# Performance work log

Hardware: AMD Instinct MI355X
Metric: run time of the kernel (lower is better)

## Reference

```python
import math
import jax, jax.numpy as jnp
import numpy as np

EPS = 1e-12
NHEAD = 12
HEAD_DIM = 64  # d_model // nhead = 768 // 12


def setup_inputs() -> dict:
    key = jax.random.key(0)
    ks = jax.random.split(key, 8)
    L, D, H = 12, 768, 2048
    B, S = 8, 1024
    std = 0.02
    return {
        "x": jax.random.normal(ks[0], (B, S, D), jnp.float32),
        "wq": jax.random.normal(ks[1], (L, D, D), jnp.float32) * std,
        "wk": jax.random.normal(ks[2], (L, D, D), jnp.float32) * std,
        "wv": jax.random.normal(ks[3], (L, D, D), jnp.float32) * std,
        "wo": jax.random.normal(ks[4], (L, D, D), jnp.float32) * std,
        "w1": jax.random.normal(ks[5], (L, H, D), jnp.float32) * std,
        "w2": jax.random.normal(ks[6], (L, D, H), jnp.float32) * std,
        "attn_norm_w": jnp.ones((L, D), jnp.float32),
        "ffn_norm_w": jnp.ones((L, D), jnp.float32),
    }


def _rmsnorm(x, w):
    # x * rsqrt(mean(x^2) + eps) * w
    return x * jax.lax.rsqrt(jnp.mean(x * x, axis=-1, keepdims=True) + EPS) * w


def _block(x, params):
    wq, wk, wv, wo, w1, w2, anw, fnw = params
    B, S, D = x.shape
    # --- attention (manual matmul-softmax-matmul, fp32 softmax) ---
    xn = _rmsnorm(x, anw)
    q = jnp.einsum('bsd,ed->bse', xn, wq).reshape(B, S, NHEAD, HEAD_DIM)
    k = jnp.einsum('bsd,ed->bse', xn, wk).reshape(B, S, NHEAD, HEAD_DIM)
    v = jnp.einsum('bsd,ed->bse', xn, wv).reshape(B, S, NHEAD, HEAD_DIM)
    scores = jnp.einsum('bqhd,bkhd->bhqk', q, k) / math.sqrt(HEAD_DIM)
    probs = jax.nn.softmax(scores.astype(jnp.float32), axis=-1).astype(x.dtype)
    attn = jnp.einsum('bhqk,bkhd->bqhd', probs, v).reshape(B, S, D)
    h = x + jnp.einsum('bsd,ed->bse', attn, wo)
    # --- FFN: w2(silu(w1(h_norm))) ---
    hn = _rmsnorm(h, fnw)
    ff = jnp.einsum('bsh,dh->bsd', jax.nn.silu(jnp.einsum('bsd,hd->bsh', hn, w1)), w2)
    return h + ff


def reference(x, wq, wk, wv, wo, w1, w2, attn_norm_w, ffn_norm_w):
    def step(carry, p):
        return _block(carry, p), None
    out, _ = jax.lax.scan(step, x, (wq, wk, wv, wo, w1, w2, attn_norm_w, ffn_norm_w))
    return out
```

## Files before the change

kernel.cpp:

```cpp
#include <hip/hip_runtime.h>
#include <stdint.h>

typedef unsigned short u16;
typedef unsigned int u32;
typedef __bf16 bf16x8 __attribute__((ext_vector_type(8)));
typedef __bf16 bf16x4 __attribute__((ext_vector_type(4)));
typedef float f32x4 __attribute__((ext_vector_type(4)));

__device__ __forceinline__ u16 f2bf(float f) {
  u32 u = __builtin_bit_cast(u32, f);
  u32 r = (u + 0x7FFFu + ((u >> 16) & 1u)) >> 16;
  return (u16)r;
}

__global__ __launch_bounds__(256)
void convert_w(const float* __restrict__ wq, const float* __restrict__ wk,
               const float* __restrict__ wv, const float* __restrict__ wo,
               const float* __restrict__ w1, const float* __restrict__ w2,
               u16* __restrict__ out) {
  size_t i = ((size_t)blockIdx.x * 256 + threadIdx.x) * 4;
  if (i >= 5505024) return;
  const float* src; size_t off;
  if (i < 589824)       { src = wq; off = i; }
  else if (i < 1179648) { src = wk; off = i - 589824; }
  else if (i < 1769472) { src = wv; off = i - 1179648; }
  else if (i < 2359296) { src = wo; off = i - 1769472; }
  else if (i < 3932160) { src = w1; off = i - 2359296; }
  else                  { src = w2; off = i - 3932160; }
  float4 v = *(const float4*)(src + off);
  u32 lo = (u32)f2bf(v.x) | ((u32)f2bf(v.y) << 16);
  u32 hi = (u32)f2bf(v.z) | ((u32)f2bf(v.w) << 16);
  *(uint2*)(out + i) = make_uint2(lo, hi);
}

__device__ __forceinline__ void rn_store4(u16* p, float4 v, float4 w, float sc) {
  u32 lo = (u32)f2bf(v.x * sc * w.x) | ((u32)f2bf(v.y * sc * w.y) << 16);
  u32 hi = (u32)f2bf(v.z * sc * w.z) | ((u32)f2bf(v.w * sc * w.w) << 16);
  *(uint2*)p = make_uint2(lo, hi);
}

__global__ __launch_bounds__(256)
void rmsnorm_k(const float* __restrict__ x, const float* __restrict__ w,
               u16* __restrict__ out) {
  const int tok = (blockIdx.x << 2) + (threadIdx.x >> 6);
  const int l = threadIdx.x & 63;
  const float* xr = x + (size_t)tok * 768;
  float4 v0 = *(const float4*)(xr + l * 4);
  float4 v1 = *(const float4*)(xr + 256 + l * 4);
  float4 v2 = *(const float4*)(xr + 512 + l * 4);
  float ss = v0.x*v0.x + v0.y*v0.y + v0.z*v0.z + v0.w*v0.w
           + v1.x*v1.x + v1.y*v1.y + v1.z*v1.z + v1.w*v1.w
           + v2.x*v2.x + v2.y*v2.y + v2.z*v2.z + v2.w*v2.w;
  ss += __shfl_xor(ss, 1);  ss += __shfl_xor(ss, 2);  ss += __shfl_xor(ss, 4);
  ss += __shfl_xor(ss, 8);  ss += __shfl_xor(ss, 16); ss += __shfl_xor(ss, 32);
  float sc = rsqrtf(ss * (1.f / 768.f) + 1e-12f);
  float4 w0 = *(const float4*)(w + l * 4);
  float4 w1v = *(const float4*)(w + 256 + l * 4);
  float4 w2v = *(const float4*)(w + 512 + l * 4);
  u16* o = out + (size_t)tok * 768;
  rn_store4(o + l * 4, v0, w0, sc);
  rn_store4(o + 256 + l * 4, v1, w1v, sc);
  rn_store4(o + 512 + l * 4, v2, w2v, sc);
}

#define GEMM_CORE(A_, W_, K_, m0_, n0_)                                             \
  for (int kt = 0; kt < (K_); kt += 64) {                                           \
    __syncthreads();                                                                \
    _Pragma("unroll")                                                               \
    for (int ii = 0; ii < 4; ++ii) {                                                \
      int issue = (w << 2) + ii;                                                    \
      int r = (issue << 3) + (l >> 3);                                              \
      int c = (l & 7) ^ (r & 7);                                                    \
      __builtin_amdgcn_global_load_lds((A_) + (size_t)((m0_) + r) * (K_) + kt + c * 8, \
                                       As + issue * 512, 16, 0, 0);                 \
      __builtin_amdgcn_global_load_lds((W_) + (size_t)((n0_) + r) * (K_) + kt + c * 8, \
                                       Ws + issue * 512, 16, 0, 0);                 \
    }                                                                               \
    __syncthreads();                                                                \
    _Pragma("unroll")                                                               \
    for (int kc = 0; kc < 2; ++kc) {                                                \
      int chunk = lg + (kc << 2);                                                   \
      bf16x8 af[4], bfr[4];                                                         \
      _Pragma("unroll")                                                             \
      for (int i = 0; i < 4; ++i) {                                                 \
        int mr = (wm << 6) + (i << 4) + ll;                                         \
        af[i] = *(const bf16x8*)((const char*)As + mr * 128 + ((chunk ^ (mr & 7)) << 4)); \
        int nr = (wn << 6) + (i << 4) + ll;                                         \
        bfr[i] = *(const bf16x8*)((const char*)Ws + nr * 128 + ((chunk ^ (nr & 7)) << 4)); \
      }                                                                             \
      _Pragma("unroll")                                                             \
      for (int i = 0; i < 4; ++i)                                                   \
        _Pragma("unroll")                                                           \
        for (int j = 0; j < 4; ++j)                                                 \
          acc[i][j] = __builtin_amdgcn_mfma_f32_16x16x32_bf16(af[i], bfr[j], acc[i][j], 0, 0, 0); \
    }                                                                               \
  }

template<int EP>
__global__ __launch_bounds__(256, 2)
void gemm_bt(const u16* __restrict__ A, const u16* __restrict__ W,
             void* __restrict__ outp, const float* __restrict__ Res,
             int M, int N, int K) {
  __shared__ __align__(16) u16 As[128 * 64];
  __shared__ __align__(16) u16 Ws[128 * 64];
  const int tid = threadIdx.x;
  const int w = tid >> 6, l = tid & 63;
  const int lg = l >> 4, ll = l & 15;
  const int ntiles = N >> 7;
  const int mt = blockIdx.x / ntiles, nt = blockIdx.x - mt * ntiles;
  const int m0 = mt << 7, n0 = nt << 7;
  const int wm = w >> 1, wn = w & 1;

  const f32x4 fz = {0.f, 0.f, 0.f, 0.f};
  f32x4 acc[4][4];
#pragma unroll
  for (int i = 0; i < 4; ++i)
#pragma unroll
    for (int j = 0; j < 4; ++j) acc[i][j] = fz;

  GEMM_CORE(A, W, K, m0, n0)

  const int g4 = lg << 2;
#pragma unroll
  for (int i = 0; i < 4; ++i) {
#pragma unroll
    for (int j = 0; j < 4; ++j) {
      int row0 = m0 + (wm << 6) + (i << 4) + g4;
      int col = n0 + (wn << 6) + (j << 4) + ll;
      f32x4 v = acc[i][j];
      if (EP == 0) {
        u16* o = (u16*)outp;
#pragma unroll
        for (int e = 0; e < 4; ++e) o[(size_t)(row0 + e) * N + col] = f2bf(v[e]);
      } else if (EP == 1) {
        float* o = (float*)outp;
#pragma unroll
        for (int e = 0; e < 4; ++e) {
          size_t idx = (size_t)(row0 + e) * N + col;
          o[idx] = Res[idx] + v[e];
        }
      } else {
        u16* o = (u16*)outp;
#pragma unroll
        for (int e = 0; e < 4; ++e) {
          float xx = v[e];
          o[(size_t)(row0 + e) * N + col] = f2bf(xx / (1.f + __expf(-xx)));
        }
      }
    }
  }
}

__global__ __launch_bounds__(256, 4)
void gemm_bt64(const u16* __restrict__ A, const u16* __restrict__ W,
               float* __restrict__ outp, const float* __restrict__ Res,
               int M, int N, int K) {
  __shared__ __align__(16) u16 As[64 * 64];
  __shared__ __align__(16) u16 Ws[128 * 64];
  const int tid = threadIdx.x;
  const int w = tid >> 6, l = tid & 63;
  const int lg = l >> 4, ll = l & 15;
  const int ntiles = N >> 7;
  const int mt = blockIdx.x / ntiles, nt = blockIdx.x - mt * ntiles;
  const int m0 = mt << 6, n0 = nt << 7;
  const int wm = w >> 1, wn = w & 1;

  const f32x4 fz = {0.f, 0.f, 0.f, 0.f};
  f32x4 acc[2][4];
#pragma unroll
  for (int i = 0; i < 2; ++i)
#pragma unroll
    for (int j = 0; j < 4; ++j) acc[i][j] = fz;

  for (int kt = 0; kt < K; kt += 64) {
    __syncthreads();
#pragma unroll
    for (int ii = 0; ii < 6; ++ii) {
      int issue = w * 6 + ii;
      if (issue < 8) {
        int r = (issue << 3) + (l >> 3);
        int c = (l & 7) ^ (r & 7);
        __builtin_amdgcn_global_load_lds(A + (size_t)(m0 + r) * K + kt + c * 8,
                                         As + issue * 512, 16, 0, 0);
      } else {
        int is2 = issue - 8;
        int r = (is2 << 3) + (l >> 3);
        int c = (l & 7) ^ (r & 7);
        __builtin_amdgcn_global_load_lds(W + (size_t)(n0 + r) * K + kt + c * 8,
                                         Ws + is2 * 512, 16, 0, 0);
      }
    }
    __syncthreads();
#pragma unroll
    for (int kc = 0; kc < 2; ++kc) {
      int chunk = lg + (kc << 2);
      bf16x8 af[2], bfr[4];
#pragma unroll
      for (int i = 0; i < 2; ++i) {
        int mr = (wm << 5) + (i << 4) + ll;
        af[i] = *(const bf16x8*)((const char*)As + mr * 128 + ((chunk ^ (mr & 7)) << 4));
      }
#pragma unroll
      for (int j = 0; j < 4; ++j) {
        int nr = (wn << 6) + (j << 4) + ll;
        bfr[j] = *(const bf16x8*)((const char*)Ws + nr * 128 + ((chunk ^ (nr & 7)) << 4));
      }
#pragma unroll
      for (int i = 0; i < 2; ++i)
#pragma unroll
        for (int j = 0; j < 4; ++j)
          acc[i][j] = __builtin_amdgcn_mfma_f32_16x16x32_bf16(af[i], bfr[j], acc[i][j], 0, 0, 0);
    }
  }

  const int g4 = lg << 2;
#pragma unroll
  for (int i = 0; i < 2; ++i) {
#pragma unroll
    for (int j = 0; j < 4; ++j) {
      int row0 = m0 + (wm << 5) + (i << 4) + g4;
      int col = n0 + (wn << 6) + (j << 4) + ll;
      f32x4 v = acc[i][j];
#pragma unroll
      for (int e = 0; e < 4; ++e) {
        size_t idx = (size_t)(row0 + e) * N + col;
        outp[idx] = Res[idx] + v[e];
      }
    }
  }
}

__global__ __launch_bounds__(256, 2)
void gemm_qkv(const u16* __restrict__ A, const u16* __restrict__ W,
              u16* __restrict__ Qo, u16* __restrict__ Ko, u16* __restrict__ Vo) {
  __shared__ __align__(16) u16 As[128 * 64];
  __shared__ __align__(16) u16 Ws[128 * 64];
  const int tid = threadIdx.x;
  const int w = tid >> 6, l = tid & 63;
  const int lg = l >> 4, ll = l & 15;
  const int mt = blockIdx.x / 18, nt = blockIdx.x - mt * 18;
  const int m0 = mt << 7, n0 = nt << 7;
  const int wm = w >> 1, wn = w & 1;
  const int K = 768;

  const f32x4 fz = {0.f, 0.f, 0.f, 0.f};
  f32x4 acc[4][4];
#pragma unroll
  for (int i = 0; i < 4; ++i)
#pragma unroll
    for (int j = 0; j < 4; ++j) acc[i][j] = fz;

  GEMM_CORE(A, W, K, m0, n0)

  const int g4 = lg << 2;
#pragma unroll
  for (int i = 0; i < 4; ++i) {
#pragma unroll
    for (int j = 0; j < 4; ++j) {
      int row0 = m0 + (wm << 6) + (i << 4) + g4;
      int col = n0 + (wn << 6) + (j << 4) + ll;
      f32x4 v = acc[i][j];
      if (nt < 12) {
        u16* o = (nt < 6) ? Qo : Ko;
        int c = (nt < 6) ? col : (col - 768);
#pragma unroll
        for (int e = 0; e < 4; ++e) o[(size_t)(row0 + e) * 768 + c] = f2bf(v[e]);
      } else {
        int c = col - 1536;
        int vrow = ((row0 >> 10) * 768) + c;
        u32 lo = (u32)f2bf(v[0]) | ((u32)f2bf(v[1]) << 16);
        u32 hi = (u32)f2bf(v[2]) | ((u32)f2bf(v[3]) << 16);
        *(uint2*)(Vo + ((size_t)vrow << 10) + (row0 & 1023)) = make_uint2(lo, hi);
      }
    }
  }
}

__global__ __launch_bounds__(256, 2)
void attn_kernel(const u16* __restrict__ Q, const u16* __restrict__ Kg,
                 const u16* __restrict__ Vt, u16* __restrict__ Og) {
  __shared__ __align__(16) u16 Ks[128 * 64];
  __shared__ __align__(16) u16 Vs[64 * 128];
  __shared__ __align__(16) __bf16 Ps[4][16 * 128];

  const int tid = threadIdx.x;
  const int w = tid >> 6, l = tid & 63;
  const int lg = l >> 4, ll = l & 15;
  const int bid = blockIdx.x;
  const int qt = bid / 96;
  const int bh = bid - qt * 96;
  const int b = bh / 12, hh = bh - b * 12;
  const float SC = 0.125f * 1.44269504f;

  bf16x8 qf[2][2];
  {
    const int tq = (b << 10) + (qt << 7) + (w << 5);
#pragma unroll
    for (int fm = 0; fm < 2; ++fm)
#pragma unroll
      for (int kc = 0; kc < 2; ++kc)
        qf[fm][kc] = *(const bf16x8*)(Q + (size_t)(tq + fm * 16 + ll) * 768 + hh * 64 + kc * 32 + lg * 8);
  }

  const f32x4 fz = {0.f, 0.f, 0.f, 0.f};
  f32x4 oacc[4][2];
#pragma unroll
  for (int i = 0; i < 4; ++i) { oacc[i][0] = fz; oacc[i][1] = fz; }
  float mrow2[2] = {-1e30f, -1e30f};
  float lrow2[2] = {0.f, 0.f};

  for (int kt = 0; kt < 8; ++kt) {
    __syncthreads();
#pragma unroll
    for (int ii = 0; ii < 4; ++ii) {
      int issue = (w << 2) + ii;
      int r = (issue << 3) + (l >> 3);
      int c = (l & 7) ^ (r & 7);
      __builtin_amdgcn_global_load_lds(
          Kg + (size_t)((b << 10) + (kt << 7) + r) * 768 + hh * 64 + c * 8,
          Ks + issue * 512, 16, 0, 0);
      int rv = (issue << 2) + (l >> 4);
      int cv = ll ^ (rv & 7);
      __builtin_amdgcn_global_load_lds(
          Vt + (size_t)((bh << 6) + rv) * 1024 + (kt << 7) + cv * 8,
          Vs + issue * 512, 16, 0, 0);
    }
    __syncthreads();

    f32x4 sa[2][8];
#pragma unroll
    for (int fm = 0; fm < 2; ++fm)
#pragma unroll
      for (int fn = 0; fn < 8; ++fn) sa[fm][fn] = fz;
#pragma unroll
    for (int kc = 0; kc < 2; ++kc) {
      int chunk = lg + (kc << 2);
      bf16x8 kb[8];
#pragma unroll
      for (int fn = 0; fn < 8; ++fn) {
        int nr = (fn << 4) + ll;
        kb[fn] = *(const bf16x8*)((const char*)Ks + nr * 128 + ((chunk ^ (nr & 7)) << 4));
      }
#pragma unroll
      for (int fm = 0; fm < 2; ++fm)
#pragma unroll
        for (int fn = 0; fn < 8; ++fn)
          sa[fm][fn] = __builtin_amdgcn_mfma_f32_16x16x32_bf16(kb[fn], qf[fm][kc], sa[fm][fn], 0, 0, 0);
    }
#pragma unroll
    for (int fm = 0; fm < 2; ++fm)
#pragma unroll
      for (int fn = 0; fn < 8; ++fn) sa[fm][fn] *= SC;

#pragma unroll
    for (int fm = 0; fm < 2; ++fm) {
      f32x4 vm = sa[fm][0];
#pragma unroll
      for (int fn = 1; fn < 8; ++fn) {
#pragma unroll
        for (int e = 0; e < 4; ++e) vm[e] = fmaxf(vm[e], sa[fm][fn][e]);
      }
      float mx = fmaxf(fmaxf(vm[0], vm[1]), fmaxf(vm[2], vm[3]));
      mx = fmaxf(mx, __shfl_xor(mx, 16));
      mx = fmaxf(mx, __shfl_xor(mx, 32));
      float mnew = fmaxf(mrow2[fm], mx);
      float scal = __builtin_amdgcn_exp2f(mrow2[fm] - mnew);

      f32x4 vsum = fz;
#pragma unroll
      for (int fn = 0; fn < 8; ++fn) {
        f32x4 p;
#pragma unroll
        for (int e = 0; e < 4; ++e) p[e] = __builtin_amdgcn_exp2f(sa[fm][fn][e] - mnew);
        vsum += p;
        bf16x4 pv4;
#pragma unroll
        for (int e = 0; e < 4; ++e) pv4[e] = (__bf16)p[e];
        int chunk = (fn << 1) + (lg >> 1);
        *(bf16x4*)((char*)&Ps[w][0] + ll * 256 + ((chunk ^ (ll & 7)) << 4) + ((lg & 1) << 3)) = pv4;
      }
      float rs = (vsum[0] + vsum[1]) + (vsum[2] + vsum[3]);
      rs += __shfl_xor(rs, 16);
      rs += __shfl_xor(rs, 32);
      lrow2[fm] = lrow2[fm] * scal + rs;
      mrow2[fm] = mnew;

      asm volatile("" ::: "memory");

#pragma unroll
      for (int fd = 0; fd < 4; ++fd) oacc[fd][fm] *= scal;

#pragma unroll
      for (int ch = 0; ch < 4; ++ch) {
        int chunk = lg + (ch << 2);
        int qr = ll;
        bf16x8 pb = *(const bf16x8*)((const char*)&Ps[w][0] + qr * 256 + ((chunk ^ (qr & 7)) << 4));
#pragma unroll
        for (int fd = 0; fd < 4; ++fd) {
          int dr = (fd << 4) + ll;
          bf16x8 av = *(const bf16x8*)((const char*)Vs + dr * 256 + ((chunk ^ (dr & 7)) << 4));
          oacc[fd][fm] = __builtin_amdgcn_mfma_f32_16x16x32_bf16(av, pb, oacc[fd][fm], 0, 0, 0);
        }
      }

      asm volatile("" ::: "memory");
    }
  }

  float inv0 = 1.f / lrow2[0];
  float inv1 = 1.f / lrow2[1];
  const int tq0 = (b << 10) + (qt << 7) + (w << 5);
#pragma unroll
  for (int fd = 0; fd < 4; ++fd) {
#pragma unroll
    for (int fo = 0; fo < 2; ++fo) {
      int q = (fo << 4) + ll;
      float inv = fo ? inv1 : inv0;
      f32x4 v = oacc[fd][fo];
      int d0 = (fd << 4) + (lg << 2);
      u16* o = Og + (size_t)(tq0 + q) * 768 + hh * 64 + d0;
      u32 lo = (u32)f2bf(v[0] * inv) | ((u32)f2bf(v[1] * inv) << 16);
      u32 hi = (u32)f2bf(v[2] * inv) | ((u32)f2bf(v[3] * inv) << 16);
      *(uint2*)o = make_uint2(lo, hi);
    }
  }
}

extern "C" void kernel_launch(void* const* d_in, const int* in_sizes, int n_in,
                              void* d_out, int out_size, void* d_ws, size_t ws_size,
                              hipStream_t stream) {
  const float* x = (const float*)d_in[0];
  const float* wq = (const float*)d_in[1];
  const float* wk = (const float*)d_in[2];
  const float* wv = (const float*)d_in[3];
  const float* wo = (const float*)d_in[4];
  const float* w1 = (const float*)d_in[5];
  const float* w2 = (const float*)d_in[6];
  const float* anw = (const float*)d_in[7];
  const float* fnw = (const float*)d_in[8];

  char* ws = (char*)d_ws;
  float* h    = (float*)(ws);
  u16* xn     = (u16*)(ws + 25165824);
  u16* qb     = (u16*)(ws + 37748736);
  u16* kb     = (u16*)(ws + 50331648);
  u16* vt     = (u16*)(ws + 62914560);
  u16* ff1    = (u16*)(ws + 75497472);
  u16* wbuf   = (u16*)(ws + 109051904);

  hipMemcpyAsync(h, x, 25165824, hipMemcpyDeviceToDevice, stream);

  for (int L = 0; L < 12; ++L) {
    convert_w<<<5376, 256, 0, stream>>>(
        wq + (size_t)L * 589824, wk + (size_t)L * 589824,
        wv + (size_t)L * 589824, wo + (size_t)L * 589824,
        w1 + (size_t)L * 1572864, w2 + (size_t)L * 1572864, wbuf);
    rmsnorm_k<<<2048, 256, 0, stream>>>(h, anw + L * 768, xn);
    gemm_qkv<<<1152, 256, 0, stream>>>(xn, wbuf, qb, kb, vt);
    attn_kernel<<<768, 256, 0, stream>>>(qb, kb, vt, qb);
    gemm_bt64<<<768, 256, 0, stream>>>(qb, wbuf + 1769472, h, h, 8192, 768, 768);
    rmsnorm_k<<<2048, 256, 0, stream>>>(h, fnw + L * 768, xn);
    gemm_bt<2><<<1024, 256, 0, stream>>>(xn, wbuf + 2359296, ff1, nullptr, 8192, 2048, 768);
    float* outw = (L == 11) ? (float*)d_out : h;
    gemm_bt64<<<768, 256, 0, stream>>>(ff1, wbuf + 3932160, outw, h, 8192, 768, 2048);
  }
}
```

Measured before the change: 2.653 ms.

## Add 256x256 pipelined SiLU GEMM for FFN up-projection and tune attention priorities

Replaces the FFN first GEMM with a new 512-thread kernel that computes 256x256 tiles. It uses a multi-stage LDS ring fed by global_load_lds, raises wave priority around the MFMA blocks, and applies SiLU in the epilogue. Separately, the attention kernel drops its explicit score-scaling pass and folds the softmax scale into the exp2 argument with an FMA, and it also wraps its MFMA sections in s_setprio. The larger tile is meant to improve operand reuse and overlap loads with compute. In exchange, the grid is only 256 blocks, which may underfill the GPU, and register pressure is higher.

New measurement: 2.672 ms. Within noise of the previous version (+0.7%).

```diff
diff --git a/kernel.cpp b/kernel.cpp
--- a/kernel.cpp
+++ b/kernel.cpp
@@ -276,6 +276,122 @@
   }
 }
 
+__global__ __launch_bounds__(512, 2)
+void gemm256_silu(const u16* __restrict__ A, const u16* __restrict__ W,
+                  u16* __restrict__ out, int M, int N, int K) {
+  __shared__ __align__(16) u16 LDS[8][8192];
+  const int tid = threadIdx.x;
+  const int w = tid >> 6, l = tid & 63;
+  const int lg = l >> 4, ll = l & 15;
+  const int wm = w >> 2, wn = w & 3;
+  const int ntiles = N >> 8;
+  const int mt = blockIdx.x / ntiles, nt = blockIdx.x - mt * ntiles;
+  const int m0 = mt << 8, n0 = nt << 8;
+  const int T = K >> 6;
+
+  const f32x4 fz = {0.f, 0.f, 0.f, 0.f};
+  f32x4 acc[8][4];
+#pragma unroll
+  for (int i = 0; i < 8; ++i)
+#pragma unroll
+    for (int j = 0; j < 4; ++j) acc[i][j] = fz;
+
+#define STG(gb, rows0, t_, kh, s)                                                    \
+  { _Pragma("unroll")                                                                \
+    for (int rr = 0; rr < 256; rr += 128) {                                          \
+      int rl = rr + (tid >> 2);                                                      \
+      int cc = (tid & 3) ^ ((rl >> 1) & 3);                                          \
+      __builtin_amdgcn_global_load_lds(                                              \
+          (gb) + (size_t)((rows0) + rl) * K + ((t_) << 6) + ((kh) << 5) + (cc << 3), \
+          &LDS[s][(rr + (w << 4)) * 32], 16, 0, 0);                                  \
+    } }
+#define BARR __builtin_amdgcn_s_barrier()
+#define VMW asm volatile("s_waitcnt vmcnt(4)" ::: "memory")
+
+  auto lda = [&](int s, int i) -> bf16x8 {
+    int r = (wm << 7) + (i << 4) + ll;
+    return *(const bf16x8*)((const char*)&LDS[s][0] + r * 64 + ((lg ^ ((r >> 1) & 3)) << 4));
+  };
+  auto ldb = [&](int s, int j) -> bf16x8 {
+    int r = (wn << 6) + (j << 4) + ll;
+    return *(const bf16x8*)((const char*)&LDS[s][0] + r * 64 + ((lg ^ ((r >> 1) & 3)) << 4));
+  };
+
+  STG(W, n0, 0, 0, 4); STG(A, m0, 0, 0, 0);
+  STG(W, n0, 0, 1, 6); STG(A, m0, 0, 1, 2);
+  STG(W, n0, 1, 0, 5); STG(A, m0, 1, 0, 1);
+  VMW; BARR;
+
+  for (int t = 0; t < T; ++t) {
+    const int par = t & 1, npar = par ^ 1;
+    bf16x8 af[4], bfr[4];
+#pragma unroll
+    for (int i = 0; i < 4; ++i) af[i] = lda(0 + par, i);
+#pragma unroll
+    for (int j = 0; j < 4; ++j) bfr[j] = ldb(4 + par, j);
+    if (t + 1 < T) STG(W, n0, t + 1, 1, 6 + npar);
+    BARR; __builtin_amdgcn_s_setprio(1);
+#pragma unroll
+    for (int i = 0; i < 4; ++i)
+#pragma unroll
+      for (int j = 0; j < 4; ++j)
+        acc[i][j] = __builtin_amdgcn_mfma_f32_16x16x32_bf16(af[i], bfr[j], acc[i][j], 0, 0, 0);
+    __builtin_amdgcn_s_setprio(0); BARR;
+#pragma unroll
+    for (int i = 0; i < 4; ++i) af[i] = lda(0 + par, 4 + i);
+    if (t + 1 < T) STG(A, m0, t + 1, 1, 2 + npar);
+    BARR; __builtin_amdgcn_s_setprio(1);
+#pragma unroll
+    for (int i = 0; i < 4; ++i)
+#pragma unroll
+      for (int j = 0; j < 4; ++j)
+        acc[4 + i][j] = __builtin_amdgcn_mfma_f32_16x16x32_bf16(af[i], bfr[j], acc[4 + i][j], 0, 0, 0);
+    __builtin_amdgcn_s_setprio(0); BARR;
+#pragma unroll
+    for (int i = 0; i < 4; ++i) af[i] = lda(2 + par, i);
+#pragma unroll
+    for (int j = 0; j < 4; ++j) bfr[j] = ldb(6 + par, j);
+    if (t + 2 < T) STG(W, n0, t + 2, 0, 4 + par);
+    BARR; __builtin_amdgcn_s_setprio(1);
+#pragma unroll
+    for (int i = 0; i < 4; ++i)
+#pragma unroll
+      for (int j = 0; j < 4; ++j)
+        acc[i][j] = __builtin_amdgcn_mfma_f32_16x16x32_bf16(af[i], bfr[j], acc[i][j], 0, 0, 0);
+    __builtin_amdgcn_s_setprio(0); BARR;
+#pragma unroll
+    for (int i = 0; i < 4; ++i) af[i] = lda(2 + par, 4 + i);
+    if (t + 2 < T) STG(A, m0, t + 2, 0, 0 + par);
+    VMW;
+    BARR; __builtin_amdgcn_s_setprio(1);
+#pragma unroll
+    for (int i = 0; i < 4; ++i)
+#pragma unroll
+      for (int j = 0; j < 4; ++j)
+        acc[4 + i][j] = __builtin_amdgcn_mfma_f32_16x16x32_bf16(af[i], bfr[j], acc[4 + i][j], 0, 0, 0);
+    __builtin_amdgcn_s_setprio(0); BARR;
+  }
+#undef STG
+#undef BARR
+#undef VMW
+
+  const int g4 = lg << 2;
+#pragma unroll
+  for (int i = 0; i < 8; ++i) {
+#pragma unroll
+    for (int j = 0; j < 4; ++j) {
+      int row0 = m0 + (wm << 7) + (i << 4) + g4;
+      int col = n0 + (wn << 6) + (j << 4) + ll;
+      f32x4 v = acc[i][j];
+#pragma unroll
+      for (int e = 0; e < 4; ++e) {
+        float xx = v[e];
+        out[(size_t)(row0 + e) * N + col] = f2bf(xx / (1.f + __expf(-xx)));
+      }
+    }
+  }
+}
+
 __global__ __launch_bounds__(256, 2)
 void attn_kernel(const u16* __restrict__ Q, const u16* __restrict__ Kg,
                  const u16* __restrict__ Vt, u16* __restrict__ Og) {
@@ -332,6 +448,7 @@
     for (int fm = 0; fm < 2; ++fm)
 #pragma unroll
       for (int fn = 0; fn < 8; ++fn) sa[fm][fn] = fz;
+    __builtin_amdgcn_s_setprio(1);
 #pragma unroll
     for (int kc = 0; kc < 2; ++kc) {
       int chunk = lg + (kc << 2);
@@ -347,10 +464,7 @@
         for (int fn = 0; fn < 8; ++fn)
           sa[fm][fn] = __builtin_amdgcn_mfma_f32_16x16x32_bf16(kb[fn], qf[fm][kc], sa[fm][fn], 0, 0, 0);
     }
-#pragma unroll
-    for (int fm = 0; fm < 2; ++fm)
-#pragma unroll
-      for (int fn = 0; fn < 8; ++fn) sa[fm][fn] *= SC;
+    __builtin_amdgcn_s_setprio(0);
 
 #pragma unroll
     for (int fm = 0; fm < 2; ++fm) {
@@ -364,14 +478,16 @@
       mx = fmaxf(mx, __shfl_xor(mx, 16));
       mx = fmaxf(mx, __shfl_xor(mx, 32));
       float mnew = fmaxf(mrow2[fm], mx);
-      float scal = __builtin_amdgcn_exp2f(mrow2[fm] - mnew);
+      float c2 = mnew * SC;
+      float scal = __builtin_amdgcn_exp2f(__builtin_fmaf(SC, mrow2[fm], -c2));
 
       f32x4 vsum = fz;
 #pragma unroll
       for (int fn = 0; fn < 8; ++fn) {
         f32x4 p;
 #pragma unroll
-        for (int e = 0; e < 4; ++e) p[e] = __builtin_amdgcn_exp2f(sa[fm][fn][e] - mnew);
+        for (int e = 0; e < 4; ++e)
+          p[e] = __builtin_amdgcn_exp2f(__builtin_fmaf(SC, sa[fm][fn][e], -c2));
         vsum += p;
         bf16x4 pv4;
 #pragma unroll
@@ -390,6 +506,7 @@
 #pragma unroll
       for (int fd = 0; fd < 4; ++fd) oacc[fd][fm] *= scal;
 
+      __builtin_amdgcn_s_setprio(1);
 #pragma unroll
       for (int ch = 0; ch < 4; ++ch) {
         int chunk = lg + (ch << 2);
@@ -402,6 +519,7 @@
           oacc[fd][fm] = __builtin_amdgcn_mfma_f32_16x16x32_bf16(av, pb, oacc[fd][fm], 0, 0, 0);
         }
       }
+      __builtin_amdgcn_s_setprio(0);
 
       asm volatile("" ::: "memory");
     }
@@ -460,7 +578,7 @@
     attn_kernel<<<768, 256, 0, stream>>>(qb, kb, vt, qb);
     gemm_bt64<<<768, 256, 0, stream>>>(qb, wbuf + 1769472, h, h, 8192, 768, 768);
     rmsnorm_k<<<2048, 256, 0, stream>>>(h, fnw + L * 768, xn);
-    gemm_bt<2><<<1024, 256, 0, stream>>>(xn, wbuf + 2359296, ff1, nullptr, 8192, 2048, 768);
+    gemm256_silu<<<256, 512, 0, stream>>>(xn, wbuf + 2359296, ff1, 8192, 2048, 768);
     float* outw = (L == 11) ? (float*)d_out : h;
     gemm_bt64<<<768, 256, 0, stream>>>(ff1, wbuf + 3932160, outw, h, 8192, 768, 2048);
   }
```
